# Optimization experiments

Hardware: AMD Instinct MI355X
Metric: run time of the kernel (lower is better)

Reference implementation:

```python
import jax, jax.numpy as jnp
import numpy as np

B, N, M, HID = 8, 384, 1536, 384
LRELU = 0.3
EPS = 1e-5


def _conv1d(x, w, b):
    # x: (B, C_in, L), w: (C_out, C_in, 3), 'same' padding
    y = jax.lax.conv_general_dilated(x, w, window_strides=(1,), padding=[(1, 1)],
                                     dimension_numbers=('NCH', 'OIH', 'NCH'))
    return y + b[None, :, None]


def _layer_norm(x, g, b):
    mu = jnp.mean(x, -1, keepdims=True)
    var = jnp.mean((x - mu) ** 2, -1, keepdims=True)
    return (x - mu) * jax.lax.rsqrt(var + EPS) * g + b


def _mlp(x, w1, b1, w2, b2):
    x = jax.nn.silu(x @ w1.T + b1)
    return jax.nn.silu(x @ w2.T + b2)


def setup_inputs() -> dict:
    key = jax.random.key(0)
    it = iter(jax.random.split(key, 48))
    def rn(shape, s):
        return jax.random.normal(next(it), shape, jnp.float32) * s
    h = HID
    inp = {}
    inp['H'] = rn((B, N, h), 1.0)
    # padding mask: last 32 phoneme slots are padding
    inp['src_mask'] = jnp.broadcast_to(jnp.arange(N)[None, :] >= N - 32, (B, N))
    inp['n_frames'] = M
    for i in (1, 2, 3):
        inp[f'w_c{i}'] = rn((h, h, 3), (1.0 / (3 * h)) ** 0.5)
        inp[f'b_c{i}'] = jnp.zeros((h,), jnp.float32)
        inp[f'g_ln{i}'] = jnp.ones((h,), jnp.float32)
        inp[f'be_ln{i}'] = jnp.zeros((h,), jnp.float32)
    inp['w_dp'] = rn((1, h), h ** -0.5)
    inp['b_dp'] = jnp.zeros((1,), jnp.float32)
    inp['w_proj'] = rn((h, h), h ** -0.5)
    inp['b_proj'] = jnp.zeros((h,), jnp.float32)
    inp['w_conv'] = rn((8, h, 3), (1.0 / (3 * h)) ** 0.5)
    inp['b_conv'] = jnp.zeros((8,), jnp.float32)
    inp['g_gn'] = jnp.ones((8,), jnp.float32)
    inp['b_gn'] = jnp.zeros((8,), jnp.float32)
    inp['wq1'] = rn((10, 10), 0.3)
    inp['bq1'] = jnp.zeros((10,), jnp.float32)
    inp['wq2'] = rn((4, 10), 0.3)
    inp['bq2'] = jnp.zeros((4,), jnp.float32)
    inp['wp1'] = rn((10, 10), 0.3)
    inp['bp1'] = jnp.zeros((10,), jnp.float32)
    inp['wp2'] = rn((2, 10), 0.3)
    inp['bp2'] = jnp.zeros((2,), jnp.float32)
    inp['w_wh'] = rn((h, 4 * h), (4 * h) ** -0.5)
    inp['b_wh'] = jnp.zeros((h,), jnp.float32)
    inp['w_wc'] = rn((h, 8), 8 ** -0.5)
    inp['b_wc'] = jnp.zeros((h,), jnp.float32)
    return inp


def reference(H, src_mask, n_frames,
              w_c1, b_c1, g_ln1, be_ln1, w_c2, b_c2, g_ln2, be_ln2,
              w_c3, b_c3, g_ln3, be_ln3, w_dp, b_dp, w_proj, b_proj,
              w_conv, b_conv, g_gn, b_gn, wq1, bq1, wq2, bq2,
              wp1, bp1, wp2, bp2, w_wh, b_wh, w_wc, b_wc):
    b, n, h = H.shape
    m = n_frames
    # ---- DurationPredictor (3 conv blocks, dropout=eval/identity) ----
    x = H
    for (wc, bc, g, be) in ((w_c1, b_c1, g_ln1, be_ln1),
                            (w_c2, b_c2, g_ln2, be_ln2),
                            (w_c3, b_c3, g_ln3, be_ln3)):
        y = _conv1d(x.transpose(0, 2, 1), wc, bc)       # (b, h, n)
        y = jax.nn.leaky_relu(y, LRELU)
        x = _layer_norm(y.transpose(0, 2, 1), g, be)    # (b, n, h)
    d = x @ w_dp.T + b_dp                               # (b, n, 1)
    d = jnp.where(src_mask[..., None], 0.0, d)[..., 0]  # (b, n)
    # ---- duration matrices S, E (eq. 6) ----
    cs = jnp.cumsum(d, 1)                                # (b, n)
    i_s = jnp.arange(1, m + 1, dtype=H.dtype)[None, :, None]  # (1, m, 1)
    csp = jnp.concatenate([jnp.zeros((b, 1), d.dtype), cs], 1)[:, :-1]
    S = i_s - csp[:, None, :]                            # (b, m, n)
    E = cs[:, None, :] - i_s                             # (b, m, n)
    # ---- project: Conv1D(Proj(H)) + GroupNorm(1,8) + SiLU ----
    p = H @ w_proj.T + b_proj                            # (b, n, h)
    p = _conv1d(p.transpose(0, 2, 1), w_conv, b_conv)    # (b, 8, n)
    mu = jnp.mean(p, (1, 2), keepdims=True)
    var = jnp.mean((p - mu) ** 2, (1, 2), keepdims=True)
    p = (p - mu) * jax.lax.rsqrt(var + EPS) * g_gn[None, :, None] + b_gn[None, :, None]
    proj = jax.nn.silu(p).transpose(0, 2, 1)             # (b, n, 8)
    # ---- concat [S, E, proj] -> (b, m, n, 10) ----
    concat = jnp.concatenate([S[..., None], E[..., None],
                              jnp.broadcast_to(proj[:, None], (b, m, n, 8))], -1)
    C = _mlp(concat, wp1, bp1, wp2, bp2)                 # (b, m, n, 2)
    W = _mlp(concat, wq1, bq1, wq2, bq2)                 # (b, m, n, 4)
    W = jnp.where(src_mask[:, None, :, None], -1e9, W)
    W = jax.nn.softmax(W, axis=2)                        # softmax over n
    Wp = W.transpose(0, 3, 1, 2)                         # (b, q, m, n)
    O_left = jnp.einsum('bqmn,bnh->bmqh', Wp, H).reshape(b, m, -1) @ w_wh.T + b_wh
    O_right = jnp.einsum('bqmn,bmnp->bmqp', Wp, C).reshape(b, m, -1) @ w_wc.T + b_wc
    return O_left + O_right
```

## Files before the change

kernel.cpp:

```cpp
#include <hip/hip_runtime.h>

#define DI __device__ __forceinline__

typedef __attribute__((ext_vector_type(8))) short bf16x8;
typedef __attribute__((ext_vector_type(4))) float f32x4;
typedef unsigned int u32;
typedef unsigned short u16;

namespace {
constexpr int Bn = 8;
constexpr int Nn = 384;
constexpr int HID = 384;
constexpr int Mn = 1536;
constexpr int NMASK = Nn - 32;
constexpr float LRELU = 0.3f;
constexpr float EPSV = 1e-5f;
constexpr int XROW = 386;

DI u16 f2bf(float f){
  union { float f; u32 i; } c; c.f = f;
  u32 r = c.i + 0x7fffu + ((c.i >> 16) & 1u);
  return (u16)(r >> 16);
}
DI u32 pk2bf(float a, float b){ return (u32)f2bf(a) | ((u32)f2bf(b) << 16); }
DI float sig_r(float x){ return __builtin_amdgcn_rcpf(1.f + __expf(-x)); }
DI float silu_f(float x){ return x * sig_r(x); }

template<int NC>
DI void wred_sum(float (&v)[NC]){
  #pragma unroll
  for (int o = 32; o; o >>= 1)
    #pragma unroll
    for (int i = 0; i < NC; i++) v[i] += __shfl_xor(v[i], o);
}
template<int NC>
DI void wred_max(float (&v)[NC]){
  #pragma unroll
  for (int o = 32; o; o >>= 1)
    #pragma unroll
    for (int i = 0; i < NC; i++) v[i] = fmaxf(v[i], __shfl_xor(v[i], o));
}

DI void gload16(const u16* g, u16* lds){
  __builtin_amdgcn_global_load_lds((const __attribute__((address_space(1))) u32*)(g),
                                   (__attribute__((address_space(3))) u32*)(lds), 16, 0, 0);
}

DI void gemm_core(const u16* __restrict__ A, int ldA, const u16* __restrict__ BT, int ldB,
                  int KT, u16* As, u16* Bs, int lane, int wid, f32x4 (&acc)[4][4])
{
  const int wr = wid >> 1, wc = wid & 1;
  const int frow = lane & 15;
  const int fch  = lane >> 4;
  const int srow = wid*32 + (lane >> 3);
  const int sch  = lane & 7;
  for (int kt = 0; kt < KT; kt++){
    const int k0 = kt*64;
    #pragma unroll
    for (int i = 0; i < 4; i++){
      int row = srow + i*8;
      int gch = sch ^ (row & 7);
      gload16(A  + (size_t)row*ldA + k0 + gch*8, As + (wid*32 + i*8)*64);
      gload16(BT + (size_t)row*ldB + k0 + gch*8, Bs + (wid*32 + i*8)*64);
    }
    __syncthreads();
    bf16x8 af[2][4], bf[2][4];
    #pragma unroll
    for (int kh = 0; kh < 2; kh++){
      #pragma unroll
      for (int mi = 0; mi < 4; mi++){
        int r = wr*64 + mi*16 + frow;
        int slot = (kh*4 + fch) ^ (r & 7);
        af[kh][mi] = *(const bf16x8*)(As + r*64 + slot*8);
      }
      #pragma unroll
      for (int ni = 0; ni < 4; ni++){
        int r = wc*64 + ni*16 + frow;
        int slot = (kh*4 + fch) ^ (r & 7);
        bf[kh][ni] = *(const bf16x8*)(Bs + r*64 + slot*8);
      }
    }
    #pragma unroll
    for (int kh = 0; kh < 2; kh++)
      #pragma unroll
      for (int mi = 0; mi < 4; mi++)
        #pragma unroll
        for (int ni = 0; ni < 4; ni++)
          acc[mi][ni] = __builtin_amdgcn_mfma_f32_16x16x32_bf16(af[kh][mi], bf[kh][ni], acc[mi][ni], 0, 0, 0);
    __syncthreads();
  }
}
}

__global__ __launch_bounds__(256) void prep_all(
    const float* __restrict__ w1, const float* __restrict__ w2, const float* __restrict__ w3,
    const float* __restrict__ wconv, const float* __restrict__ w_wh,
    const float* __restrict__ w_proj, const float* __restrict__ H,
    u16* __restrict__ wkT, float* __restrict__ wconvT, u16* __restrict__ Wcat,
    u16* __restrict__ xpad1, u16* __restrict__ xpad2)
{
  int g = blockIdx.x*256 + threadIdx.x;
  const int S0 = 3*HID*HID;
  if (g < S0){
    int l = g / (HID*HID);
    int r = g % (HID*HID);
    const float* w = (l==0) ? w1 : ((l==1) ? w2 : w3);
    float a = w[r*3+0], b = w[r*3+1], c = w[r*3+2];
    u16* base = wkT + (size_t)l*3*HID*HID + r;
    base[0]         = f2bf(a);
    base[HID*HID]   = f2bf(b);
    base[2*HID*HID] = f2bf(c);
    return;
  }
  g -= S0;
  const int S1 = 8*HID;
  if (g < S1){
    int c = g / HID, ci = g % HID;
    const float* src = wconv + ((size_t)c*HID + ci)*3;
    wconvT[(c*3+0)*HID + ci] = src[0];
    wconvT[(c*3+1)*HID + ci] = src[1];
    wconvT[(c*3+2)*HID + ci] = src[2];
    return;
  }
  g -= S1;
  const int S2 = 1920*HID/4;
  if (g < S2){
    int e0 = g*4;
    int n = e0 / HID, kk = e0 % HID;
    float4 v;
    if (n < 1536){
      int q = n / HID, h = n % HID;
      v = *(const float4*)(w_wh + (size_t)h*1536 + q*HID + kk);
    } else {
      v = *(const float4*)(w_proj + (size_t)(n-1536)*HID + kk);
    }
    *(ushort4*)(Wcat + e0) = make_ushort4(f2bf(v.x), f2bf(v.y), f2bf(v.z), f2bf(v.w));
    return;
  }
  g -= S2;
  const int S3 = Bn*XROW*(HID/4);
  if (g < S3){
    int b = g / (XROW*96);
    int r = g % (XROW*96);
    int row = r / 96, c4 = r % 96;
    ushort4 o = make_ushort4(0,0,0,0);
    if (row >= 1 && row <= Nn){
      float4 v = *(const float4*)(H + (((size_t)b*Nn) + row - 1)*HID + c4*4);
      o = make_ushort4(f2bf(v.x), f2bf(v.y), f2bf(v.z), f2bf(v.w));
    }
    *(ushort4*)(xpad1 + ((size_t)b*XROW + row)*HID + c4*4) = o;
    return;
  }
  g -= S3;
  if (g < Bn*2*96){
    int b = g / (2*96);
    int r = g % (2*96);
    int row = (r / 96) ? (XROW-1) : 0;
    int c4 = r % 96;
    *(ushort4*)(xpad2 + ((size_t)b*XROW + row)*HID + c4*4) = make_ushort4(0,0,0,0);
  }
}

__global__ __launch_bounds__(256) void conv_mfma(
    const u16* __restrict__ xpad, const u16* __restrict__ wkT, float* __restrict__ y)
{
  __shared__ u16 As[128*64];
  __shared__ u16 Bs[128*64];
  const int t = threadIdx.x, lane = t & 63, wid = t >> 6;
  const int mt = blockIdx.x;
  const int nt = blockIdx.y;
  const int b = mt / 3, jt = mt % 3;
  f32x4 acc[4][4];
  #pragma unroll
  for (int i = 0; i < 4; i++)
    #pragma unroll
    for (int jj = 0; jj < 4; jj++) acc[i][jj] = f32x4{0.f,0.f,0.f,0.f};
  #pragma unroll
  for (int k = 0; k < 3; k++)
    gemm_core(xpad + ((size_t)b*XROW + jt*128 + k)*HID, HID,
              wkT + (size_t)k*HID*HID + (size_t)nt*128*HID, HID, HID/64,
              As, Bs, lane, wid, acc);
  const int wr = wid >> 1, wc = wid & 1;
  const int r0 = jt*128 + wr*64 + (lane >> 4)*4;
  const int c0 = nt*128 + wc*64 + (lane & 15);
  #pragma unroll
  for (int mi = 0; mi < 4; mi++)
    #pragma unroll
    for (int ni = 0; ni < 4; ni++)
      #pragma unroll
      for (int r = 0; r < 4; r++)
        y[((size_t)b*Nn + r0 + mi*16 + r)*HID + c0 + ni*16] = acc[mi][ni][r];
}

__global__ __launch_bounds__(256) void ln_row_kern(
    const float* __restrict__ y, const float* __restrict__ bc, const float* __restrict__ g,
    const float* __restrict__ be, u16* __restrict__ xpad_out,
    const float* __restrict__ w_dp, const float* __restrict__ b_dp, float* __restrict__ d_out)
{
  const int row = (blockIdx.x*256 + threadIdx.x) >> 6;
  const int lane = threadIdx.x & 63;
  const int b = row / Nn, n = row % Nn;
  const int c0 = lane*6;
  const float* rp = y + (size_t)row*HID + c0;
  float v[6];
  {
    float2 a0 = *(const float2*)(rp);
    float2 a1 = *(const float2*)(rp + 2);
    float2 a2 = *(const float2*)(rp + 4);
    v[0]=a0.x; v[1]=a0.y; v[2]=a1.x; v[3]=a1.y; v[4]=a2.x; v[5]=a2.y;
  }
  #pragma unroll
  for (int e = 0; e < 6; e++){
    float x = v[e] + bc[c0+e];
    v[e] = x >= 0.f ? x : LRELU*x;
  }
  float s2[2] = {0.f, 0.f};
  #pragma unroll
  for (int e = 0; e < 6; e++){ s2[0] += v[e]; s2[1] += v[e]*v[e]; }
  wred_sum<2>(s2);
  const float mu = s2[0] * (1.f/HID);
  const float var = s2[1] * (1.f/HID) - mu*mu;
  const float rs = rsqrtf(var + EPSV);
  #pragma unroll
  for (int e = 0; e < 6; e++) v[e] = (v[e] - mu)*rs*g[c0+e] + be[c0+e];
  if (xpad_out){
    u32* dst = (u32*)(xpad_out + ((size_t)b*XROW + 1 + n)*HID + c0);
    dst[0] = pk2bf(v[0], v[1]);
    dst[1] = pk2bf(v[2], v[3]);
    dst[2] = pk2bf(v[4], v[5]);
  }
  if (d_out){
    float dv[1] = {0.f};
    #pragma unroll
    for (int e = 0; e < 6; e++) dv[0] += v[e]*w_dp[c0+e];
    wred_sum<1>(dv);
    if (lane == 0) d_out[row] = (n >= NMASK) ? 0.f : dv[0] + b_dp[0];
  }
}

__global__ __launch_bounds__(64) void scan_kern(const float* __restrict__ d, float* __restrict__ cs)
{
  const int b = blockIdx.x, lane = threadIdx.x;
  const float* dp = d + b*Nn + lane*6;
  float v[6];
  #pragma unroll
  for (int e = 0; e < 6; e++) v[e] = dp[e];
  #pragma unroll
  for (int e = 1; e < 6; e++) v[e] += v[e-1];
  float incl = v[5];
  #pragma unroll
  for (int o = 1; o < 64; o <<= 1){
    float u = __shfl_up(incl, o);
    if (lane >= o) incl += u;
  }
  const float pre = incl - v[5];
  float* cp = cs + b*(Nn+1);
  if (lane == 0) cp[0] = 0.f;
  #pragma unroll
  for (int e = 0; e < 6; e++) cp[1 + lane*6 + e] = v[e] + pre;
}

__global__ __launch_bounds__(256) void hproj_mfma(
    const u16* __restrict__ xpad1, const u16* __restrict__ Wcat,
    const float* __restrict__ b_proj, u16* __restrict__ KtT, float* __restrict__ p1)
{
  __shared__ u16 As[128*64];
  __shared__ u16 Bs[128*64];
  const int t = threadIdx.x, lane = t & 63, wid = t >> 6;
  const int mt = blockIdx.x;
  const int nt = blockIdx.y;
  const int b = mt / 3, jt = mt % 3;
  f32x4 acc[4][4];
  #pragma unroll
  for (int i = 0; i < 4; i++)
    #pragma unroll
    for (int jj = 0; jj < 4; jj++) acc[i][jj] = f32x4{0.f,0.f,0.f,0.f};
  gemm_core(xpad1 + ((size_t)b*XROW + 1 + jt*128)*HID, HID,
            Wcat + (size_t)nt*128*HID, HID, HID/64, As, Bs, lane, wid, acc);
  const int wr = wid >> 1, wc = wid & 1;
  const int j0 = jt*128 + wr*64 + (lane >> 4)*4;
  if (nt < 12){
    const int q = nt / 3;
    const int hb = (nt % 3)*128 + wc*64 + (lane & 15);
    #pragma unroll
    for (int mi = 0; mi < 4; mi++){
      #pragma unroll
      for (int ni = 0; ni < 4; ni++){
        int h = hb + ni*16;
        int j = j0 + mi*16;
        ushort4 pk = make_ushort4(f2bf(acc[mi][ni][0]), f2bf(acc[mi][ni][1]),
                                  f2bf(acc[mi][ni][2]), f2bf(acc[mi][ni][3]));
        *(ushort4*)(KtT + (size_t)b*589824 + (size_t)h*1536 + q*HID + j) = pk;
      }
    }
  } else {
    const int hb = (nt - 12)*128 + wc*64 + (lane & 15);
    #pragma unroll
    for (int mi = 0; mi < 4; mi++){
      #pragma unroll
      for (int ni = 0; ni < 4; ni++){
        int h = hb + ni*16;
        float bp = b_proj[h];
        #pragma unroll
        for (int r = 0; r < 4; r++){
          int j = j0 + mi*16 + r;
          p1[((size_t)b*Nn + j)*HID + h] = acc[mi][ni][r] + bp;
        }
      }
    }
  }
}

__global__ __launch_bounds__(256) void projc8_kern(
    const float* __restrict__ p1, const float* __restrict__ wconvT,
    const float* __restrict__ b_conv, float* __restrict__ p8tmp, float* __restrict__ partials)
{
  __shared__ float xs[34][388];
  __shared__ float sc[8];
  const int b  = blockIdx.x / 12;
  const int ch = blockIdx.x % 12;
  const int n0 = ch*32;
  const int t  = threadIdx.x;
  for (int idx = t; idx < 34*96; idx += 256){
    int r = idx / 96, c4 = idx % 96;
    int n = n0 - 1 + r;
    float4 v = (n >= 0 && n < Nn) ? *(const float4*)(p1 + ((size_t)b*Nn + n)*HID + c4*4)
                                  : make_float4(0.f,0.f,0.f,0.f);
    *(float4*)(&xs[r][c4*4]) = v;
  }
  __syncthreads();
  const int nl = t >> 3, c = t & 7;
  const float* wb = wconvT + (size_t)c*3*HID;
  float pc = b_conv[c];
  for (int ci = 0; ci < HID; ci += 4){
    float4 w0 = *(const float4*)(wb + ci);
    float4 w1 = *(const float4*)(wb + HID + ci);
    float4 w2 = *(const float4*)(wb + 2*HID + ci);
    float4 x0 = *(const float4*)(&xs[nl][ci]);
    float4 x1 = *(const float4*)(&xs[nl+1][ci]);
    float4 x2 = *(const float4*)(&xs[nl+2][ci]);
    pc += w0.x*x0.x + w0.y*x0.y + w0.z*x0.z + w0.w*x0.w
        + w1.x*x1.x + w1.y*x1.y + w1.z*x1.z + w1.w*x1.w
        + w2.x*x2.x + w2.y*x2.y + w2.z*x2.z + w2.w*x2.w;
  }
  p8tmp[((size_t)b*Nn + n0 + nl)*8 + c] = pc;
  float sv[2] = {pc, pc*pc};
  #pragma unroll
  for (int o = 32; o; o >>= 1){ sv[0] += __shfl_down(sv[0], o); sv[1] += __shfl_down(sv[1], o); }
  if ((t & 63) == 0){ sc[(t>>6)*2] = sv[0]; sc[(t>>6)*2+1] = sv[1]; }
  __syncthreads();
  if (t == 0){
    float s = 0.f, q = 0.f;
    #pragma unroll
    for (int w = 0; w < 4; w++){ s += sc[w*2]; q += sc[w*2+1]; }
    partials[blockIdx.x*2] = s; partials[blockIdx.x*2+1] = q;
  }
}

__global__ __launch_bounds__(Nn) void gnwprep_kern(
    const float* __restrict__ p8tmp, const float* __restrict__ partials,
    const float* __restrict__ g_gn, const float* __restrict__ b_gn,
    const float* __restrict__ cs,
    const float* __restrict__ wq1, const float* __restrict__ bq1,
    const float* __restrict__ wp1, const float* __restrict__ bp1,
    float* __restrict__ baseQP)
{
  const int b = blockIdx.x, j = threadIdx.x;
  float s = 0.f, q = 0.f;
  #pragma unroll
  for (int i = 0; i < 12; i++){ s += partials[(b*12+i)*2]; q += partials[(b*12+i)*2+1]; }
  const float inv = 1.f/(8.f*Nn);
  const float mu = s*inv;
  const float var = q*inv - mu*mu;
  const float rs = rsqrtf(var + EPSV);
  float4 v0 = *(const float4*)(p8tmp + ((size_t)b*Nn + j)*8);
  float4 v1 = *(const float4*)(p8tmp + ((size_t)b*Nn + j)*8 + 4);
  float p8[8] = {v0.x,v0.y,v0.z,v0.w,v1.x,v1.y,v1.z,v1.w};
  #pragma unroll
  for (int c = 0; c < 8; c++) p8[c] = silu_f((p8[c]-mu)*rs*g_gn[c] + b_gn[c]);
  const float csp = cs[b*(Nn+1) + j];
  const float csj = cs[b*(Nn+1) + j + 1];
  #pragma unroll
  for (int i = 0; i < 10; i++){
    float v = bq1[i] - wq1[i*10+0]*csp + wq1[i*10+1]*csj;
    float u = bp1[i] - wp1[i*10+0]*csp + wp1[i*10+1]*csj;
    #pragma unroll
    for (int k = 0; k < 8; k++){
      v += wq1[i*10+2+k]*p8[k];
      u += wp1[i*10+2+k]*p8[k];
    }
    baseQP[((size_t)b*20 + i)*Nn + j]      = v;
    baseQP[((size_t)b*20 + 10 + i)*Nn + j] = u;
  }
}

__global__ __launch_bounds__(512) void wsoft_kern(
    const float* __restrict__ baseQP,
    const float* __restrict__ wq1, const float* __restrict__ wq2, const float* __restrict__ bq2,
    const float* __restrict__ wp1, const float* __restrict__ wp2, const float* __restrict__ bp2,
    u16* __restrict__ Wt, float* __restrict__ R)
{
  __shared__ float bs[20*Nn];
  const int t = threadIdx.x, lane = t & 63, wid = t >> 6;
  const int g = blockIdx.x*8 + wid;
  const int bb = (blockIdx.x*8) / Mn;
  const int m = g - bb*Mn;
  for (int idx = t; idx < 20*Nn/4; idx += 512)
    *(float4*)(&bs[idx*4]) = *(const float4*)(baseQP + (size_t)bb*20*Nn + idx*4);
  __syncthreads();
  const float fi = (float)(m + 1);
  float w4s[6][4], c2s[6][2];
  #pragma unroll
  for (int s = 0; s < 6; s++){
    const int j = s*64 + lane;
    float h1[10];
    #pragma unroll
    for (int i = 0; i < 10; i++){
      float sl = wq1[i*10+0] - wq1[i*10+1];
      h1[i] = silu_f(fmaf(sl, fi, bs[i*Nn + j]));
    }
    const bool masked = (s == 5) && (lane >= 32);
    #pragma unroll
    for (int o = 0; o < 4; o++){
      float v = bq2[o];
      #pragma unroll
      for (int k = 0; k < 10; k++) v += wq2[o*10+k]*h1[k];
      w4s[s][o] = masked ? -1e9f : silu_f(v);
    }
    #pragma unroll
    for (int i = 0; i < 10; i++){
      float sl = wp1[i*10+0] - wp1[i*10+1];
      h1[i] = silu_f(fmaf(sl, fi, bs[(10+i)*Nn + j]));
    }
    #pragma unroll
    for (int o = 0; o < 2; o++){
      float v = bp2[o];
      #pragma unroll
      for (int k = 0; k < 10; k++) v += wp2[o*10+k]*h1[k];
      c2s[s][o] = silu_f(v);
    }
  }
  float mx[4] = {-3e38f,-3e38f,-3e38f,-3e38f};
  #pragma unroll
  for (int s = 0; s < 6; s++)
    #pragma unroll
    for (int o = 0; o < 4; o++) mx[o] = fmaxf(mx[o], w4s[s][o]);
  wred_max<4>(mx);
  float sm[4] = {0.f,0.f,0.f,0.f};
  #pragma unroll
  for (int s = 0; s < 6; s++)
    #pragma unroll
    for (int o = 0; o < 4; o++){ w4s[s][o] = __expf(w4s[s][o] - mx[o]); sm[o] += w4s[s][o]; }
  wred_sum<4>(sm);
  float inv[4];
  #pragma unroll
  for (int o = 0; o < 4; o++) inv[o] = __builtin_amdgcn_rcpf(sm[o]);
  float pr[8] = {0.f,0.f,0.f,0.f,0.f,0.f,0.f,0.f};
  #pragma unroll
  for (int s = 0; s < 6; s++){
    const int j = s*64 + lane;
    #pragma unroll
    for (int o = 0; o < 4; o++){
      float wn = w4s[s][o]*inv[o];
      Wt[(size_t)g*1536 + o*Nn + j] = f2bf(wn);
      pr[o*2+0] += wn*c2s[s][0];
      pr[o*2+1] += wn*c2s[s][1];
    }
  }
  wred_sum<8>(pr);
  if (lane == 0){
    #pragma unroll
    for (int i = 0; i < 8; i++) R[(size_t)g*8 + i] = pr[i];
  }
}

__global__ __launch_bounds__(256) void outgemm_mfma(
    const u16* __restrict__ Wt, const u16* __restrict__ KtT,
    const float* __restrict__ R, const float* __restrict__ b_wh,
    const float* __restrict__ w_wc, const float* __restrict__ b_wc,
    float* __restrict__ out)
{
  __shared__ u16 As[128*64];
  __shared__ u16 Bs[128*64];
  const int t = threadIdx.x, lane = t & 63, wid = t >> 6;
  const int mt = blockIdx.x;
  const int nt = blockIdx.y;
  const int b  = blockIdx.z;
  f32x4 acc[4][4];
  #pragma unroll
  for (int i = 0; i < 4; i++)
    #pragma unroll
    for (int jj = 0; jj < 4; jj++) acc[i][jj] = f32x4{0.f,0.f,0.f,0.f};
  gemm_core(Wt + (size_t)b*Mn*1536 + (size_t)mt*128*1536, 1536,
            KtT + (size_t)b*589824 + (size_t)nt*128*1536, 1536, 24,
            As, Bs, lane, wid, acc);
  const int wr = wid >> 1, wc = wid & 1;
  float bbv[4], wcv[4][8];
  #pragma unroll
  for (int ni = 0; ni < 4; ni++){
    int h = nt*128 + wc*64 + ni*16 + (lane & 15);
    bbv[ni] = b_wh[h] + b_wc[h];
    float4 a0 = *(const float4*)(w_wc + (size_t)h*8);
    float4 a1 = *(const float4*)(w_wc + (size_t)h*8 + 4);
    wcv[ni][0]=a0.x; wcv[ni][1]=a0.y; wcv[ni][2]=a0.z; wcv[ni][3]=a0.w;
    wcv[ni][4]=a1.x; wcv[ni][5]=a1.y; wcv[ni][6]=a1.z; wcv[ni][7]=a1.w;
  }
  #pragma unroll
  for (int mi = 0; mi < 4; mi++){
    #pragma unroll
    for (int r = 0; r < 4; r++){
      int m = mt*128 + wr*64 + mi*16 + (lane >> 4)*4 + r;
      const float* Rp = R + ((size_t)b*Mn + m)*8;
      float4 r0 = *(const float4*)(Rp);
      float4 r1 = *(const float4*)(Rp + 4);
      float R8[8] = {r0.x,r0.y,r0.z,r0.w,r1.x,r1.y,r1.z,r1.w};
      #pragma unroll
      for (int ni = 0; ni < 4; ni++){
        int h = nt*128 + wc*64 + ni*16 + (lane & 15);
        float v = acc[mi][ni][r] + bbv[ni];
        #pragma unroll
        for (int p = 0; p < 8; p++) v += R8[p]*wcv[ni][p];
        out[((size_t)b*Mn + m)*HID + h] = v;
      }
    }
  }
}

extern "C" void kernel_launch(void* const* d_in, const int* in_sizes, int n_in,
                              void* d_out, int out_size, void* d_ws, size_t ws_size,
                              hipStream_t stream) {
  (void)in_sizes; (void)n_in; (void)out_size; (void)ws_size;
  const float* Hin    = (const float*)d_in[0];
  const float* w_c1   = (const float*)d_in[3];
  const float* b_c1   = (const float*)d_in[4];
  const float* g1     = (const float*)d_in[5];
  const float* be1    = (const float*)d_in[6];
  const float* w_c2   = (const float*)d_in[7];
  const float* b_c2   = (const float*)d_in[8];
  const float* g2     = (const float*)d_in[9];
  const float* be2    = (const float*)d_in[10];
  const float* w_c3   = (const float*)d_in[11];
  const float* b_c3   = (const float*)d_in[12];
  const float* g3     = (const float*)d_in[13];
  const float* be3    = (const float*)d_in[14];
  const float* w_dp   = (const float*)d_in[15];
  const float* b_dp   = (const float*)d_in[16];
  const float* w_proj = (const float*)d_in[17];
  const float* b_proj = (const float*)d_in[18];
  const float* w_conv = (const float*)d_in[19];
  const float* b_conv = (const float*)d_in[20];
  const float* g_gn   = (const float*)d_in[21];
  const float* b_gn   = (const float*)d_in[22];
  const float* wq1    = (const float*)d_in[23];
  const float* bq1    = (const float*)d_in[24];
  const float* wq2    = (const float*)d_in[25];
  const float* bq2    = (const float*)d_in[26];
  const float* wp1    = (const float*)d_in[27];
  const float* bp1    = (const float*)d_in[28];
  const float* wp2    = (const float*)d_in[29];
  const float* bp2    = (const float*)d_in[30];
  const float* w_wh   = (const float*)d_in[31];
  const float* b_wh   = (const float*)d_in[32];
  const float* w_wc   = (const float*)d_in[33];
  const float* b_wc   = (const float*)d_in[34];

  char* ws = (char*)d_ws;
  u16*   Wt      = (u16*)(ws + 0);
  u16*   wkT     = (u16*)(ws + 0);
  float* wconvT  = (float*)(ws + 2654208);
  u16*   Wcat    = (u16*)(ws + 2691072);
  u16*   KtT     = (u16*)(ws + 37748736);
  u16*   xpad1   = (u16*)(ws + 47185920);
  float* baseQP  = (float*)(ws + 47185920);
  u16*   xpad2   = (u16*)(ws + 49557504);
  float* R_w     = (float*)(ws + 49557504);
  float* y_buf   = (float*)(ws + 51929088);
  float* p1      = y_buf;
  float* p8tmp   = (float*)(ws + 56647680);
  float* partials= (float*)(ws + 56745984);
  float* d_w     = (float*)(ws + 56747008);
  float* cs_w    = (float*)(ws + 56759296);

  const int PREP_T = 3*HID*HID + 8*HID + 1920*HID/4 + Bn*XROW*(HID/4) + Bn*2*(HID/4);
  prep_all<<<(PREP_T + 255)/256, 256, 0, stream>>>(w_c1, w_c2, w_c3, w_conv, w_wh, w_proj, Hin,
                                                   wkT, wconvT, Wcat, xpad1, xpad2);

  conv_mfma<<<dim3(24,3), 256, 0, stream>>>(xpad1, wkT,             y_buf);
  ln_row_kern<<<Bn*Nn/4, 256, 0, stream>>>(y_buf, b_c1, g1, be1, xpad2, nullptr, nullptr, nullptr);
  conv_mfma<<<dim3(24,3), 256, 0, stream>>>(xpad2, wkT + 3*HID*HID, y_buf);
  ln_row_kern<<<Bn*Nn/4, 256, 0, stream>>>(y_buf, b_c2, g2, be2, xpad2, nullptr, nullptr, nullptr);
  conv_mfma<<<dim3(24,3), 256, 0, stream>>>(xpad2, wkT + 6*HID*HID, y_buf);
  ln_row_kern<<<Bn*Nn/4, 256, 0, stream>>>(y_buf, b_c3, g3, be3, nullptr, w_dp, b_dp, d_w);
  scan_kern<<<Bn, 64, 0, stream>>>(d_w, cs_w);

  hproj_mfma<<<dim3(24,15), 256, 0, stream>>>(xpad1, Wcat, b_proj, KtT, p1);

  projc8_kern<<<Bn*12, 256, 0, stream>>>(p1, wconvT, b_conv, p8tmp, partials);
  gnwprep_kern<<<Bn, Nn, 0, stream>>>(p8tmp, partials, g_gn, b_gn, cs_w, wq1, bq1, wp1, bp1, baseQP);

  wsoft_kern<<<Bn*Mn/8, 512, 0, stream>>>(baseQP, wq1, wq2, bq2, wp1, wp2, bp2, Wt, R_w);

  outgemm_mfma<<<dim3(12,3,8), 256, 0, stream>>>(Wt, KtT, R_w, b_wh, w_wc, b_wc, (float*)d_out);
}
```

Baseline: 225.0 us.

## Split conv taps across grid z and fold prefix scan into gnwprep

Each conv layer's three kernel taps now run as separate blocks along grid z. Each tap writes its own partial output slice, and the layer-norm kernel sums the three slices when it reads them. This triples the block count from 72 to 216 so the GPU's compute units are better occupied. The cost is three times the fp32 intermediate writes and reads. The standalone scan kernel is also removed and the cumulative sum is computed inside gnwprep with a shared-memory Hillis-Steele scan, saving one launch.

```diff
diff --git a/kernel.cpp b/kernel.cpp
--- a/kernel.cpp
+++ b/kernel.cpp
@@ -16,6 +16,7 @@
 constexpr float LRELU = 0.3f;
 constexpr float EPSV = 1e-5f;
 constexpr int XROW = 386;
+constexpr int YSZ = 3072*HID;
 
 DI u16 f2bf(float f){
   union { float f; u32 i; } c; c.f = f;
@@ -162,24 +163,24 @@
 }
 
 __global__ __launch_bounds__(256) void conv_mfma(
-    const u16* __restrict__ xpad, const u16* __restrict__ wkT, float* __restrict__ y)
+    const u16* __restrict__ xpad, const u16* __restrict__ wkT, float* __restrict__ ys)
 {
   __shared__ u16 As[128*64];
   __shared__ u16 Bs[128*64];
   const int t = threadIdx.x, lane = t & 63, wid = t >> 6;
   const int mt = blockIdx.x;
   const int nt = blockIdx.y;
+  const int kz = blockIdx.z;
   const int b = mt / 3, jt = mt % 3;
+  float* y = ys + (size_t)kz*YSZ;
   f32x4 acc[4][4];
   #pragma unroll
   for (int i = 0; i < 4; i++)
     #pragma unroll
     for (int jj = 0; jj < 4; jj++) acc[i][jj] = f32x4{0.f,0.f,0.f,0.f};
-  #pragma unroll
-  for (int k = 0; k < 3; k++)
-    gemm_core(xpad + ((size_t)b*XROW + jt*128 + k)*HID, HID,
-              wkT + (size_t)k*HID*HID + (size_t)nt*128*HID, HID, HID/64,
-              As, Bs, lane, wid, acc);
+  gemm_core(xpad + ((size_t)b*XROW + jt*128 + kz)*HID, HID,
+            wkT + (size_t)kz*HID*HID + (size_t)nt*128*HID, HID, HID/64,
+            As, Bs, lane, wid, acc);
   const int wr = wid >> 1, wc = wid & 1;
   const int r0 = jt*128 + wr*64 + (lane >> 4)*4;
   const int c0 = nt*128 + wc*64 + (lane & 15);
@@ -193,7 +194,7 @@
 }
 
 __global__ __launch_bounds__(256) void ln_row_kern(
-    const float* __restrict__ y, const float* __restrict__ bc, const float* __restrict__ g,
+    const float* __restrict__ ys, const float* __restrict__ bc, const float* __restrict__ g,
     const float* __restrict__ be, u16* __restrict__ xpad_out,
     const float* __restrict__ w_dp, const float* __restrict__ b_dp, float* __restrict__ d_out)
 {
@@ -201,13 +202,15 @@
   const int lane = threadIdx.x & 63;
   const int b = row / Nn, n = row % Nn;
   const int c0 = lane*6;
-  const float* rp = y + (size_t)row*HID + c0;
-  float v[6];
-  {
-    float2 a0 = *(const float2*)(rp);
-    float2 a1 = *(const float2*)(rp + 2);
-    float2 a2 = *(const float2*)(rp + 4);
-    v[0]=a0.x; v[1]=a0.y; v[2]=a1.x; v[3]=a1.y; v[4]=a2.x; v[5]=a2.y;
+  const float* rp = ys + (size_t)row*HID + c0;
+  float v[6] = {0.f,0.f,0.f,0.f,0.f,0.f};
+  #pragma unroll
+  for (int sl = 0; sl < 3; sl++){
+    const float* p = rp + (size_t)sl*YSZ;
+    float2 a0 = *(const float2*)(p);
+    float2 a1 = *(const float2*)(p + 2);
+    float2 a2 = *(const float2*)(p + 4);
+    v[0]+=a0.x; v[1]+=a0.y; v[2]+=a1.x; v[3]+=a1.y; v[4]+=a2.x; v[5]+=a2.y;
   }
   #pragma unroll
   for (int e = 0; e < 6; e++){
@@ -236,28 +239,6 @@
     wred_sum<1>(dv);
     if (lane == 0) d_out[row] = (n >= NMASK) ? 0.f : dv[0] + b_dp[0];
   }
-}
-
-__global__ __launch_bounds__(64) void scan_kern(const float* __restrict__ d, float* __restrict__ cs)
-{
-  const int b = blockIdx.x, lane = threadIdx.x;
-  const float* dp = d + b*Nn + lane*6;
-  float v[6];
-  #pragma unroll
-  for (int e = 0; e < 6; e++) v[e] = dp[e];
-  #pragma unroll
-  for (int e = 1; e < 6; e++) v[e] += v[e-1];
-  float incl = v[5];
-  #pragma unroll
-  for (int o = 1; o < 64; o <<= 1){
-    float u = __shfl_up(incl, o);
-    if (lane >= o) incl += u;
-  }
-  const float pre = incl - v[5];
-  float* cp = cs + b*(Nn+1);
-  if (lane == 0) cp[0] = 0.f;
-  #pragma unroll
-  for (int e = 0; e < 6; e++) cp[1 + lane*6 + e] = v[e] + pre;
 }
 
 __global__ __launch_bounds__(256) void hproj_mfma(
@@ -360,12 +341,26 @@
 __global__ __launch_bounds__(Nn) void gnwprep_kern(
     const float* __restrict__ p8tmp, const float* __restrict__ partials,
     const float* __restrict__ g_gn, const float* __restrict__ b_gn,
-    const float* __restrict__ cs,
+    const float* __restrict__ d,
     const float* __restrict__ wq1, const float* __restrict__ bq1,
     const float* __restrict__ wp1, const float* __restrict__ bp1,
     float* __restrict__ baseQP)
 {
+  __shared__ float sb[Nn];
   const int b = blockIdx.x, j = threadIdx.x;
+  const float dj = d[b*Nn + j];
+  float incl = dj;
+  sb[j] = incl;
+  __syncthreads();
+  for (int off = 1; off < Nn; off <<= 1){
+    float add = (j >= off) ? sb[j - off] : 0.f;
+    __syncthreads();
+    incl += add;
+    sb[j] = incl;
+    __syncthreads();
+  }
+  const float csj = incl;
+  const float csp = incl - dj;
   float s = 0.f, q = 0.f;
   #pragma unroll
   for (int i = 0; i < 12; i++){ s += partials[(b*12+i)*2]; q += partials[(b*12+i)*2+1]; }
@@ -378,8 +373,6 @@
   float p8[8] = {v0.x,v0.y,v0.z,v0.w,v1.x,v1.y,v1.z,v1.w};
   #pragma unroll
   for (int c = 0; c < 8; c++) p8[c] = silu_f((p8[c]-mu)*rs*g_gn[c] + b_gn[c]);
-  const float csp = cs[b*(Nn+1) + j];
-  const float csj = cs[b*(Nn+1) + j + 1];
   #pragma unroll
   for (int i = 0; i < 10; i++){
     float v = bq1[i] - wq1[i*10+0]*csp + wq1[i*10+1]*csj;
@@ -569,34 +562,32 @@
   u16*   wkT     = (u16*)(ws + 0);
   float* wconvT  = (float*)(ws + 2654208);
   u16*   Wcat    = (u16*)(ws + 2691072);
+  float* ys      = (float*)(ws + 4194304);
   u16*   KtT     = (u16*)(ws + 37748736);
   u16*   xpad1   = (u16*)(ws + 47185920);
   float* baseQP  = (float*)(ws + 47185920);
   u16*   xpad2   = (u16*)(ws + 49557504);
   float* R_w     = (float*)(ws + 49557504);
-  float* y_buf   = (float*)(ws + 51929088);
-  float* p1      = y_buf;
+  float* p1      = (float*)(ws + 51929088);
   float* p8tmp   = (float*)(ws + 56647680);
   float* partials= (float*)(ws + 56745984);
   float* d_w     = (float*)(ws + 56747008);
-  float* cs_w    = (float*)(ws + 56759296);
 
   const int PREP_T = 3*HID*HID + 8*HID + 1920*HID/4 + Bn*XROW*(HID/4) + Bn*2*(HID/4);
   prep_all<<<(PREP_T + 255)/256, 256, 0, stream>>>(w_c1, w_c2, w_c3, w_conv, w_wh, w_proj, Hin,
                                                    wkT, wconvT, Wcat, xpad1, xpad2);
 
-  conv_mfma<<<dim3(24,3), 256, 0, stream>>>(xpad1, wkT,             y_buf);
-  ln_row_kern<<<Bn*Nn/4, 256, 0, stream>>>(y_buf, b_c1, g1, be1, xpad2, nullptr, nullptr, nullptr);
-  conv_mfma<<<dim3(24,3), 256, 0, stream>>>(xpad2, wkT + 3*HID*HID, y_buf);
-  ln_row_kern<<<Bn*Nn/4, 256, 0, stream>>>(y_buf, b_c2, g2, be2, xpad2, nullptr, nullptr, nullptr);
-  conv_mfma<<<dim3(24,3), 256, 0, stream>>>(xpad2, wkT + 6*HID*HID, y_buf);
-  ln_row_kern<<<Bn*Nn/4, 256, 0, stream>>>(y_buf, b_c3, g3, be3, nullptr, w_dp, b_dp, d_w);
-  scan_kern<<<Bn, 64, 0, stream>>>(d_w, cs_w);
+  conv_mfma<<<dim3(24,3,3), 256, 0, stream>>>(xpad1, wkT,             ys);
+  ln_row_kern<<<Bn*Nn/4, 256, 0, stream>>>(ys, b_c1, g1, be1, xpad2, nullptr, nullptr, nullptr);
+  conv_mfma<<<dim3(24,3,3), 256, 0, stream>>>(xpad2, wkT + 3*HID*HID, ys);
+  ln_row_kern<<<Bn*Nn/4, 256, 0, stream>>>(ys, b_c2, g2, be2, xpad2, nullptr, nullptr, nullptr);
+  conv_mfma<<<dim3(24,3,3), 256, 0, stream>>>(xpad2, wkT + 6*HID*HID, ys);
+  ln_row_kern<<<Bn*Nn/4, 256, 0, stream>>>(ys, b_c3, g3, be3, nullptr, w_dp, b_dp, d_w);
 
   hproj_mfma<<<dim3(24,15), 256, 0, stream>>>(xpad1, Wcat, b_proj, KtT, p1);
 
   projc8_kern<<<Bn*12, 256, 0, stream>>>(p1, wconvT, b_conv, p8tmp, partials);
-  gnwprep_kern<<<Bn, Nn, 0, stream>>>(p8tmp, partials, g_gn, b_gn, cs_w, wq1, bq1, wp1, bp1, baseQP);
+  gnwprep_kern<<<Bn, Nn, 0, stream>>>(p8tmp, partials, g_gn, b_gn, d_w, wq1, bq1, wp1, bp1, baseQP);
 
   wsoft_kern<<<Bn*Mn/8, 512, 0, stream>>>(baseQP, wq1, wq2, bq2, wp1, wp2, bp2, Wt, R_w);
 
```

After: 204.9 us. -8.9%, faster.
